# Performance work log

Measured on AMD Instinct MI355X. Metric: run time of the kernel, lower is better.

Reference implementation:

```python
import math
import jax, jax.numpy as jnp
from jax import lax
import numpy as np

# Defaults of DifferenceOfGaussians
MIN_SIGMA, SIGMA_RATIO, MAX_SIGMA, TRUNCATE = 1.0, 1.2, 10.0, 4.0
K = int(np.log(MAX_SIGMA / MIN_SIGMA) / np.log(SIGMA_RATIO) + 1)  # 13
SIGMAS_NP = np.array([MIN_SIGMA * SIGMA_RATIO ** i for i in range(K + 1)], np.float32)
MAX_RADIUS = int(TRUNCATE * SIGMAS_NP.max() + 0.5)  # 43
THRESHOLD = 0.001
PAD = (3 - 1) // 2  # footprint=3 -> padding 1
MAX_PEAKS = 32768  # fixed cap for jit-compatible nonzero


def _build_pyramid_weight():
    """Replicates GaussianSmoothing kernels (incl. its exp(-(d/(2s))^2) form),
    zero-padded to the common 87x87 support. Shape [K+1, 1, 87, 87] (OIHW)."""
    ksz = 2 * MAX_RADIUS + 1
    W = np.zeros((K + 1, 1, ksz, ksz), np.float32)
    for i, s in enumerate(SIGMAS_NP):
        r = int(TRUNCATE * s + 0.5)
        n = 2 * r + 1
        g = np.arange(n, dtype=np.float32)
        mean = (n - 1) / 2.0
        g1 = (1.0 / (s * math.sqrt(2 * math.pi))) * np.exp(-(((g - mean) / (2.0 * s)) ** 2))
        k2 = np.outer(g1, g1)
        k2 /= k2.sum()
        p = MAX_RADIUS - r
        W[i, 0, p:p + n, p:p + n] = k2
    return jnp.asarray(W)


def setup_inputs() -> dict:
    key = jax.random.key(0)
    x = jax.random.uniform(key, (1, 1, 512, 512), dtype=jnp.float32)
    weight = _build_pyramid_weight()            # [14, 1, 87, 87]
    sigma_list = jnp.asarray(SIGMAS_NP)         # [14]
    return {"x": x, "weight": weight, "sigma_list": sigma_list}


def reference(x, weight, sigma_list):
    # ConstantPad2d(max_radius) then VALID conv -> output spatially == input
    xp = jnp.pad(x, ((0, 0), (0, 0), (MAX_RADIUS, MAX_RADIUS), (MAX_RADIUS, MAX_RADIUS)))
    g = lax.conv_general_dilated(
        xp, weight, window_strides=(1, 1), padding='VALID',
        dimension_numbers=('NCHW', 'OIHW', 'NCHW'))[0]        # [K+1, H, W]
    # DoG stack scaled by sigma: [K, H, W]
    dog = (g[:-1] - g[1:]) * sigma_list[:K][:, None, None]
    # 3D max-pool, kernel 3, stride 1, pad 1 (same shape)
    image_max = lax.reduce_window(dog, -jnp.inf, lax.max,
                                  (3, 3, 3), (1, 1, 1), [(PAD, PAD)] * 3)
    mask = (dog == image_max) & (dog > THRESHOLD)
    # exclude_border: zero out PAD-wide borders along every dim (incl. scale dim)
    mask = mask.at[:PAD].set(False).at[-PAD:].set(False)
    mask = mask.at[:, :PAD].set(False).at[:, -PAD:].set(False)
    mask = mask.at[:, :, :PAD].set(False).at[:, :, -PAD:].set(False)
    # fixed-size nonzero (padded rows have indices (0,0,0); (0,*,*) is always
    # masked out by border exclusion, so real peaks never collide with padding)
    s_idx, y_idx, x_idx = jnp.nonzero(mask, size=MAX_PEAKS, fill_value=0)
    local_maxima = jnp.stack([sigma_list[s_idx],
                              y_idx.astype(jnp.float32),
                              x_idx.astype(jnp.float32)], axis=1)  # [MAX_PEAKS, 3]
    return local_maxima
```

## Files before the change

kernel.cpp:

```cpp
#include <hip/hip_runtime.h>
#include <hip/hip_bf16.h>


#define OFF_H    0
#define OFF_DOG  18350080
#define OFF_BITS 31981568
#define OFF_GCNT 32407552

#define HROWS 640
#define HPAD  43
#define NSIG 13
#define MAXPEAKS 32768

__device__ __forceinline__ void make_w(float s, double sgn, double* wl, int lane) {
    int r = (int)(4.0f * s + 0.5f);
    int n = 2 * r + 1;
    double v0 = 0.0, v1 = 0.0;
    double sd = (double)s;
    if (lane < n) {
        double d = (double)(lane - r), q = d / (2.0 * sd);
        v0 = exp(-q * q);
    }
    if (lane + 64 < n) {
        double d = (double)(lane + 64 - r), q = d / (2.0 * sd);
        v1 = exp(-q * q);
    }
    double part = v0 + v1;
    for (int m = 1; m < 64; m <<= 1) part += __shfl_xor(part, m);
    double inv = sgn / part;
    wl[lane] = v0 * inv;
    if (lane + 64 < 96) wl[lane + 64] = v1 * inv;
}

__global__ __launch_bounds__(256) void hpass(const float* __restrict__ x,
                                             const float* __restrict__ sigma_list,
                                             float* __restrict__ h) {
    const int i = 13 - blockIdx.y;
    const int t = threadIdx.x;
    float s = sigma_list[i];
    int r = (int)(4.0f * s + 0.5f);
    int n = 2 * r + 1;
    int nceil = (n + 15) & ~15;

    __shared__ double wl[96];
    if (t < 64) make_w(s, +1.0, wl, t);

    {
        float* hp = h + i * (HROWS * 512);
        for (int k = t; k < 688; k += 256) {
            int f = blockIdx.x * 688 + k;
            int g = f >> 9, xc = f & 511;
            int row = (g < HPAD) ? g : (g + 512);
            hp[row * 512 + xc] = 0.0f;
        }
    }

    __shared__ float rowp[8][648];
    int y8 = blockIdx.x * 8;
    for (int rr = 0; rr < 8; ++rr)
        for (int k = t; k < 608; k += 256) {
            int gx = k - 43;
            float val = ((unsigned)gx < 512u) ? x[(y8 + rr) * 512 + gx] : 0.0f;
            rowp[rr][k + (k >> 4)] = val;
        }
    __syncthreads();

    int tsub = t & 31, row = t >> 5;
    int xb = tsub * 16;
    int P0 = 43 - r + xb;
    double acc[16], win[16];
#pragma unroll
    for (int j = 0; j < 16; ++j) acc[j] = 0.0;
#pragma unroll
    for (int sl = 0; sl < 16; ++sl) {
        int p = P0 + sl;
        win[sl] = (double)rowp[row][p + (p >> 4)];
    }
    for (int dc = 0; dc < nceil; dc += 16) {
#pragma unroll
        for (int k = 0; k < 16; ++k) {
            double wd = wl[dc + k];
#pragma unroll
            for (int j = 0; j < 16; ++j)
                acc[j] = fma(wd, win[(k + j) & 15], acc[j]);
            int p = P0 + dc + k + 16;
            win[k] = (double)rowp[row][p + (p >> 4)];
        }
    }
    float* hp = h + (i * HROWS + HPAD + y8 + row) * 512 + xb;
#pragma unroll
    for (int j = 0; j < 16; ++j) hp[j] = (float)acc[j];
}

__device__ __forceinline__ void conv_acc(const float* __restrict__ bp,
                                         int nceil, const double* __restrict__ wl,
                                         double (&acc)[16]) {
    double win[32];
#pragma unroll
    for (int sl = 0; sl < 32; ++sl) win[sl] = (double)bp[sl * 512];
    int dc = 0;
    for (; dc + 32 <= nceil; dc += 32) {
        const float* rp = bp + (dc + 32) * 512;
#pragma unroll
        for (int k = 0; k < 16; ++k) {
            double wd = wl[dc + k];
#pragma unroll
            for (int j = 0; j < 16; ++j)
                acc[j] = fma(wd, win[(k + j) & 31], acc[j]);
            win[k] = (double)rp[k * 512];
        }
#pragma unroll
        for (int k = 16; k < 32; ++k) {
            double wd = wl[dc + k];
#pragma unroll
            for (int j = 0; j < 16; ++j)
                acc[j] = fma(wd, win[(k + j) & 31], acc[j]);
            win[k] = (double)rp[k * 512];
        }
    }
    if (nceil & 16) {
        const float* rp = bp + (dc + 32) * 512;
#pragma unroll
        for (int k = 0; k < 16; ++k) {
            double wd = wl[dc + k];
#pragma unroll
            for (int j = 0; j < 16; ++j)
                acc[j] = fma(wd, win[(k + j) & 31], acc[j]);
            win[k] = (double)rp[k * 512];
        }
    }
}

__global__ __launch_bounds__(64) void vdog(const float* __restrict__ h,
                                           const float* __restrict__ sigma_list,
                                           float* __restrict__ dog) {
    const int di = 12 - blockIdx.z;
    const int lane = threadIdx.x;
    const int x = blockIdx.x * 64 + lane;
    const int y0 = blockIdx.y * 16;
    float s0 = sigma_list[di], s1 = sigma_list[di + 1];
    int r0 = (int)(4.0f * s0 + 0.5f), n0 = 2 * r0 + 1, nc0 = (n0 + 15) & ~15;
    int r1 = (int)(4.0f * s1 + 0.5f), n1 = 2 * r1 + 1, nc1 = (n1 + 15) & ~15;
    __shared__ double wl0[96], wl1[96];
    make_w(s0, +1.0, wl0, lane);
    make_w(s1, -1.0, wl1, lane);
    __syncthreads();
    double acc[16];
#pragma unroll
    for (int j = 0; j < 16; ++j) acc[j] = 0.0;
    const float* hp0 = h + di * (HROWS * 512);
    conv_acc(hp0 + (HPAD + y0 - r0) * 512 + x, nc0, wl0, acc);
    const float* hp1 = hp0 + HROWS * 512;
    conv_acc(hp1 + (HPAD + y0 - r1) * 512 + x, nc1, wl1, acc);
    double sg = (double)s0;
    float* dp = dog + (di * 512 + y0) * 512 + x;
#pragma unroll
    for (int j = 0; j < 16; ++j) dp[j * 512] = (float)(acc[j] * sg);
}

__global__ __launch_bounds__(512) void detect(const float* __restrict__ dog,
                                              unsigned long long* __restrict__ rowbits,
                                              int* __restrict__ gcnt) {
    const int s = blockIdx.y + 1;
    const int y0 = blockIdx.x * 8;
    const int group = s * 64 + blockIdx.x;
    const int t = threadIdx.x;
    const int w = t >> 6, lane = t & 63;

    float pm[10], vcen[8];
#pragma unroll
    for (int k = 0; k < 8; ++k) vcen[k] = 0.0f;
#pragma unroll
    for (int q = 0; q < 10; ++q) {
        int yy = y0 - 1 + q;
        float m = -3.0e38f;
        if ((unsigned)yy < 512u) {
            float a = dog[((s - 1) * 512 + yy) * 512 + t];
            float b = dog[(s * 512 + yy) * 512 + t];
            float c = dog[((s + 1) * 512 + yy) * 512 + t];
            m = fmaxf(a, fmaxf(b, c));
            if (q >= 1 && q <= 8) vcen[q - 1] = b;
        }
        pm[q] = m;
    }
    __shared__ float cml[8][512];
    __shared__ int cnt[8][8];
#pragma unroll
    for (int k = 0; k < 8; ++k)
        cml[k][t] = fmaxf(pm[k], fmaxf(pm[k + 1], pm[k + 2]));
    __syncthreads();
#pragma unroll
    for (int k = 0; k < 8; ++k) {
        int y = y0 + k;
        bool peak = false;
        if (t >= 1 && t <= 510 && y >= 1 && y <= 510) {
            float v = vcen[k];
            if (v > 0.001f) {
                float mx = fmaxf(cml[k][t - 1], fmaxf(cml[k][t], cml[k][t + 1]));
                peak = (v >= mx);
            }
        }
        unsigned long long m = __ballot(peak);
        if (lane == 0) {
            rowbits[(s * 512 + y) * 8 + w] = m;
            cnt[k][w] = __popcll(m);
        }
    }
    __syncthreads();
    if (t == 0) {
        int c = 0;
#pragma unroll
        for (int k = 0; k < 8; ++k)
#pragma unroll
            for (int q = 0; q < 8; ++q) c += cnt[k][q];
        gcnt[group] = c;
    }
}

__global__ __launch_bounds__(512) void emit(const unsigned long long* __restrict__ rowbits,
                                            const int* __restrict__ gcnt,
                                            const float* __restrict__ sigma_list,
                                            float* __restrict__ out) {
    const int b = blockIdx.x;
    const int s = b >> 6;
    const int y0 = (b & 63) * 8;
    const int t = threadIdx.x;
    const int lane = t & 63;
    const bool interior = (s >= 1 && s <= 11);

    __shared__ unsigned long long m[64];
    __shared__ int pre[64];
    __shared__ int redA[512], redB[512];

    if (interior && t < 64)
        m[t] = rowbits[(s * 512 + y0 + (t >> 3)) * 8 + (t & 7)];

    int pa = 0, pb = 0;
    {
        int c0 = (t >= 64) ? gcnt[t] : 0;
        int i1 = t + 512;
        int c1 = (i1 < 768) ? gcnt[i1] : 0;
        pb = c0 + c1;
        if (t < b) pa += c0;
        if (i1 < b) pa += c1;
    }
    redA[t] = pa;
    redB[t] = pb;
    __syncthreads();
    for (int off = 256; off > 0; off >>= 1) {
        if (t < off) { redA[t] += redA[t + off]; redB[t] += redB[t + off]; }
        __syncthreads();
    }
    int gbase = redA[0];
    int tot = min(redB[0], MAXPEAKS);

    if (interior) {
        if (t < 64) {
            int wc = (int)__popcll(m[t]);
            int inc = wc;
            for (int off = 1; off < 64; off <<= 1) {
                int v = __shfl_up(inc, off);
                if (lane >= off) inc += v;
            }
            pre[t] = inc - wc;
        }
        __syncthreads();

#pragma unroll
        for (int k = 0; k < 8; ++k) {
            int widx = k * 8 + (t >> 6);
            unsigned long long mw = m[widx];
            if ((mw >> lane) & 1ull) {
                int pos = gbase + pre[widx] + (int)__popcll(mw & ((1ull << lane) - 1ull));
                if (pos < MAXPEAKS) {
                    out[pos * 3 + 0] = sigma_list[s];
                    out[pos * 3 + 1] = (float)(y0 + k);
                    out[pos * 3 + 2] = (float)t;
                }
            }
        }
    }

    int idx = b * 512 + t;
    if (idx < MAXPEAKS && idx >= tot) {
        out[idx * 3 + 0] = sigma_list[0];
        out[idx * 3 + 1] = 0.0f;
        out[idx * 3 + 2] = 0.0f;
    }
}

extern "C" void kernel_launch(void* const* d_in, const int* in_sizes, int n_in,
                              void* d_out, int out_size, void* d_ws, size_t ws_size,
                              hipStream_t stream) {
    const float* x     = (const float*)d_in[0];
    const float* sigma = (const float*)d_in[2];
    float* out = (float*)d_out;

    char* ws = (char*)d_ws;
    float* h                     = (float*)(ws + OFF_H);
    float* dog                   = (float*)(ws + OFF_DOG);
    unsigned long long* rowbits  = (unsigned long long*)(ws + OFF_BITS);
    int* gcnt                    = (int*)(ws + OFF_GCNT);

    hpass<<<dim3(64, 14), 256, 0, stream>>>(x, sigma, h);
    vdog<<<dim3(8, 32, 13), 64, 0, stream>>>(h, sigma, dog);
    detect<<<dim3(64, 11), 512, 0, stream>>>(dog, rowbits, gcnt);
    emit<<<832, 512, 0, stream>>>(rowbits, gcnt, sigma, out);
}
```

Baseline: 111.2 us.

## Fuse vertical DoG convolution with 3D peak detection in one kernel

Replaces the separate vertical-conv DoG kernel and the detection kernel with a single kernel. Each block computes the vertical Gaussian passes for four adjacent scales over 18 rows with halo, forms the three DoG planes in registers and runs the max-pool test directly. This removes the DoG intermediate buffer round trip through memory and one launch. In exchange, each scale's vertical convolutions are recomputed for neighbouring scale blocks, and register pressure rises. The horizontal padding grows to 44 rows to cover the extra halo row.

```diff
diff --git a/kernel.cpp b/kernel.cpp
--- a/kernel.cpp
+++ b/kernel.cpp
@@ -3,13 +3,11 @@
 
 
 #define OFF_H    0
-#define OFF_DOG  18350080
-#define OFF_BITS 31981568
-#define OFF_GCNT 32407552
+#define OFF_BITS 18350080
+#define OFF_GCNT 18776064
 
 #define HROWS 640
-#define HPAD  43
-#define NSIG 13
+#define HPAD  44
 #define MAXPEAKS 32768
 
 __device__ __forceinline__ void make_w(float s, double sgn, double* wl, int lane) {
@@ -47,8 +45,8 @@
 
     {
         float* hp = h + i * (HROWS * 512);
-        for (int k = t; k < 688; k += 256) {
-            int f = blockIdx.x * 688 + k;
+        for (int k = t; k < 704; k += 256) {
+            int f = blockIdx.x * 704 + k;
             int g = f >> 9, xc = f & 511;
             int row = (g < HPAD) ? g : (g + 512);
             hp[row * 512 + xc] = 0.0f;
@@ -92,128 +90,125 @@
     for (int j = 0; j < 16; ++j) hp[j] = (float)acc[j];
 }
 
-__device__ __forceinline__ void conv_acc(const float* __restrict__ bp,
-                                         int nceil, const double* __restrict__ wl,
-                                         double (&acc)[16]) {
+__device__ __forceinline__ void conv18(const float* __restrict__ bp,
+                                       int nceil, const double* __restrict__ wl,
+                                       double (&g)[18]) {
     double win[32];
 #pragma unroll
     for (int sl = 0; sl < 32; ++sl) win[sl] = (double)bp[sl * 512];
+#pragma unroll
+    for (int j = 0; j < 18; ++j) g[j] = 0.0;
     int dc = 0;
     for (; dc + 32 <= nceil; dc += 32) {
         const float* rp = bp + (dc + 32) * 512;
 #pragma unroll
+        for (int k = 0; k < 32; ++k) {
+            double wd = wl[dc + k];
+#pragma unroll
+            for (int j = 0; j < 18; ++j)
+                g[j] = fma(wd, win[(k + j) & 31], g[j]);
+            win[k] = (double)rp[k * 512];
+        }
+    }
+    if (nceil & 16) {
+        const float* rp = bp + (dc + 32) * 512;
+#pragma unroll
         for (int k = 0; k < 16; ++k) {
             double wd = wl[dc + k];
 #pragma unroll
-            for (int j = 0; j < 16; ++j)
-                acc[j] = fma(wd, win[(k + j) & 31], acc[j]);
+            for (int j = 0; j < 18; ++j)
+                g[j] = fma(wd, win[(k + j) & 31], g[j]);
             win[k] = (double)rp[k * 512];
         }
-#pragma unroll
-        for (int k = 16; k < 32; ++k) {
-            double wd = wl[dc + k];
-#pragma unroll
-            for (int j = 0; j < 16; ++j)
-                acc[j] = fma(wd, win[(k + j) & 31], acc[j]);
-            win[k] = (double)rp[k * 512];
-        }
-    }
-    if (nceil & 16) {
-        const float* rp = bp + (dc + 32) * 512;
-#pragma unroll
-        for (int k = 0; k < 16; ++k) {
-            double wd = wl[dc + k];
-#pragma unroll
-            for (int j = 0; j < 16; ++j)
-                acc[j] = fma(wd, win[(k + j) & 31], acc[j]);
-            win[k] = (double)rp[k * 512];
-        }
-    }
-}
-
-__global__ __launch_bounds__(64) void vdog(const float* __restrict__ h,
-                                           const float* __restrict__ sigma_list,
-                                           float* __restrict__ dog) {
-    const int di = 12 - blockIdx.z;
-    const int lane = threadIdx.x;
-    const int x = blockIdx.x * 64 + lane;
-    const int y0 = blockIdx.y * 16;
-    float s0 = sigma_list[di], s1 = sigma_list[di + 1];
-    int r0 = (int)(4.0f * s0 + 0.5f), n0 = 2 * r0 + 1, nc0 = (n0 + 15) & ~15;
-    int r1 = (int)(4.0f * s1 + 0.5f), n1 = 2 * r1 + 1, nc1 = (n1 + 15) & ~15;
-    __shared__ double wl0[96], wl1[96];
-    make_w(s0, +1.0, wl0, lane);
-    make_w(s1, -1.0, wl1, lane);
-    __syncthreads();
-    double acc[16];
-#pragma unroll
-    for (int j = 0; j < 16; ++j) acc[j] = 0.0;
-    const float* hp0 = h + di * (HROWS * 512);
-    conv_acc(hp0 + (HPAD + y0 - r0) * 512 + x, nc0, wl0, acc);
-    const float* hp1 = hp0 + HROWS * 512;
-    conv_acc(hp1 + (HPAD + y0 - r1) * 512 + x, nc1, wl1, acc);
-    double sg = (double)s0;
-    float* dp = dog + (di * 512 + y0) * 512 + x;
-#pragma unroll
-    for (int j = 0; j < 16; ++j) dp[j * 512] = (float)(acc[j] * sg);
-}
-
-__global__ __launch_bounds__(512) void detect(const float* __restrict__ dog,
-                                              unsigned long long* __restrict__ rowbits,
-                                              int* __restrict__ gcnt) {
-    const int s = blockIdx.y + 1;
-    const int y0 = blockIdx.x * 8;
-    const int group = s * 64 + blockIdx.x;
+    }
+}
+
+__global__ __launch_bounds__(512) void vdet(const float* __restrict__ h,
+                                            const float* __restrict__ sigma_list,
+                                            unsigned long long* __restrict__ rowbits,
+                                            int* __restrict__ gcnt) {
+    const int s = 11 - blockIdx.y;
+    const int yt = blockIdx.x;
+    const int y0 = yt * 16;
     const int t = threadIdx.x;
-    const int w = t >> 6, lane = t & 63;
-
-    float pm[10], vcen[8];
-#pragma unroll
-    for (int k = 0; k < 8; ++k) vcen[k] = 0.0f;
-#pragma unroll
-    for (int q = 0; q < 10; ++q) {
-        int yy = y0 - 1 + q;
-        float m = -3.0e38f;
-        if ((unsigned)yy < 512u) {
-            float a = dog[((s - 1) * 512 + yy) * 512 + t];
-            float b = dog[(s * 512 + yy) * 512 + t];
-            float c = dog[((s + 1) * 512 + yy) * 512 + t];
-            m = fmaxf(a, fmaxf(b, c));
-            if (q >= 1 && q <= 8) vcen[q - 1] = b;
-        }
-        pm[q] = m;
-    }
-    __shared__ float cml[8][512];
-    __shared__ int cnt[8][8];
-#pragma unroll
-    for (int k = 0; k < 8; ++k)
-        cml[k][t] = fmaxf(pm[k], fmaxf(pm[k + 1], pm[k + 2]));
-    __syncthreads();
-#pragma unroll
-    for (int k = 0; k < 8; ++k) {
+    const int wv = t >> 6, lane = t & 63;
+
+    __shared__ double wl[4][96];
+    __shared__ float rmAll[512][17];
+    __shared__ int cnt[16][8];
+
+    if (wv < 4) make_w(sigma_list[s - 1 + wv], +1.0, wl[wv], lane);
+    __syncthreads();
+
+    int r[4], nc[4];
+#pragma unroll
+    for (int p = 0; p < 4; ++p) {
+        float sp = sigma_list[s - 1 + p];
+        r[p] = (int)(4.0f * sp + 0.5f);
+        nc[p] = (2 * r[p] + 16) & ~15;
+    }
+    const int PS = HROWS * 512;
+    const float* hb = h + (s - 1) * PS;
+
+    double A[18], B[18];
+    float pm3[18], vcen[16];
+
+    conv18(hb + (HPAD + y0 - 1 - r[0]) * 512 + t, nc[0], wl[0], A);
+    conv18(hb + PS + (HPAD + y0 - 1 - r[1]) * 512 + t, nc[1], wl[1], B);
+    {
+        double sg = (double)sigma_list[s - 1];
+#pragma unroll
+        for (int j = 0; j < 18; ++j) pm3[j] = (float)((A[j] - B[j]) * sg);
+    }
+    conv18(hb + 2 * PS + (HPAD + y0 - 1 - r[2]) * 512 + t, nc[2], wl[2], A);
+    {
+        double sg = (double)sigma_list[s];
+#pragma unroll
+        for (int j = 0; j < 18; ++j) {
+            float d = (float)((B[j] - A[j]) * sg);
+            pm3[j] = fmaxf(pm3[j], d);
+            if (j >= 1 && j <= 16) vcen[j - 1] = d;
+        }
+    }
+    conv18(hb + 3 * PS + (HPAD + y0 - 1 - r[3]) * 512 + t, nc[3], wl[3], B);
+    {
+        double sg = (double)sigma_list[s + 1];
+#pragma unroll
+        for (int j = 0; j < 18; ++j)
+            pm3[j] = fmaxf(pm3[j], (float)((A[j] - B[j]) * sg));
+    }
+
+#pragma unroll
+    for (int k = 0; k < 16; ++k)
+        rmAll[t][k] = fmaxf(pm3[k], fmaxf(pm3[k + 1], pm3[k + 2]));
+    __syncthreads();
+
+#pragma unroll
+    for (int k = 0; k < 16; ++k) {
         int y = y0 + k;
         bool peak = false;
         if (t >= 1 && t <= 510 && y >= 1 && y <= 510) {
             float v = vcen[k];
             if (v > 0.001f) {
-                float mx = fmaxf(cml[k][t - 1], fmaxf(cml[k][t], cml[k][t + 1]));
+                float mx = fmaxf(rmAll[t - 1][k],
+                           fmaxf(rmAll[t][k], rmAll[t + 1][k]));
                 peak = (v >= mx);
             }
         }
         unsigned long long m = __ballot(peak);
         if (lane == 0) {
-            rowbits[(s * 512 + y) * 8 + w] = m;
-            cnt[k][w] = __popcll(m);
-        }
-    }
-    __syncthreads();
-    if (t == 0) {
+            rowbits[(s * 512 + y) * 8 + wv] = m;
+            cnt[k][wv] = __popcll(m);
+        }
+    }
+    __syncthreads();
+    if (t < 2) {
         int c = 0;
 #pragma unroll
         for (int k = 0; k < 8; ++k)
 #pragma unroll
-            for (int q = 0; q < 8; ++q) c += cnt[k][q];
-        gcnt[group] = c;
+            for (int q = 0; q < 8; ++q) c += cnt[t * 8 + k][q];
+        gcnt[s * 64 + yt * 2 + t] = c;
     }
 }
 
@@ -298,12 +293,10 @@
 
     char* ws = (char*)d_ws;
     float* h                     = (float*)(ws + OFF_H);
-    float* dog                   = (float*)(ws + OFF_DOG);
     unsigned long long* rowbits  = (unsigned long long*)(ws + OFF_BITS);
     int* gcnt                    = (int*)(ws + OFF_GCNT);
 
     hpass<<<dim3(64, 14), 256, 0, stream>>>(x, sigma, h);
-    vdog<<<dim3(8, 32, 13), 64, 0, stream>>>(h, sigma, dog);
-    detect<<<dim3(64, 11), 512, 0, stream>>>(dog, rowbits, gcnt);
+    vdet<<<dim3(32, 11), 512, 0, stream>>>(h, sigma, rowbits, gcnt);
     emit<<<832, 512, 0, stream>>>(rowbits, gcnt, sigma, out);
 }
```

After: 118.4 us. 6.5% more time.
